# Optimization experiments

Measured on AMD Instinct MI355X. Metric: run time of the kernel, lower is better.

## Reference

```python
import jax, jax.numpy as jnp
import numpy as np

S = 2048      # seq_len
E = 1024      # embedding_size
H = 16        # attn_head
D = E // H    # per-head dim = 64
EPS = 1e-5


def _layernorm(x, g, b):
    mu = jnp.mean(x, axis=-1, keepdims=True)
    var = jnp.var(x, axis=-1, keepdims=True)
    return (x - mu) * jax.lax.rsqrt(var + EPS) * g + b


def setup_inputs() -> dict:
    key = jax.random.key(0)
    ks = jax.random.split(key, 16)
    s = 1.0 / np.sqrt(E)
    inp = {
        "x_word_emb": jax.random.normal(ks[0], (S, E), jnp.float32),
        "x_pos_emb": jax.random.normal(ks[1], (S, E), jnp.float32),
        # stacked per-head projections: weight [H, E, D], bias [H, D]
        "Wq": jax.random.uniform(ks[2], (H, E, D), jnp.float32, -s, s),
        "bq": jax.random.uniform(ks[3], (H, D), jnp.float32, -s, s),
        "Wk": jax.random.uniform(ks[4], (H, E, D), jnp.float32, -s, s),
        "bk": jax.random.uniform(ks[5], (H, D), jnp.float32, -s, s),
        "Wv": jax.random.uniform(ks[6], (H, E, D), jnp.float32, -s, s),
        "bv": jax.random.uniform(ks[7], (H, D), jnp.float32, -s, s),
        "W0": jax.random.uniform(ks[8], (E, E), jnp.float32, -s, s),
        "b0": jax.random.uniform(ks[9], (E,), jnp.float32, -s, s),
        "g1": jnp.ones((E,), jnp.float32),
        "be1": jnp.zeros((E,), jnp.float32),
        "W1": jax.random.uniform(ks[10], (4 * E, E), jnp.float32, -s, s),
        "b1": jax.random.uniform(ks[11], (4 * E,), jnp.float32, -s, s),
        "W2": jax.random.uniform(ks[12], (E, 4 * E), jnp.float32, -1.0 / np.sqrt(4 * E), 1.0 / np.sqrt(4 * E)),
        "b2": jax.random.uniform(ks[13], (E,), jnp.float32, -1.0 / np.sqrt(4 * E), 1.0 / np.sqrt(4 * E)),
        "g2": jnp.ones((E,), jnp.float32),
        "be2": jnp.zeros((E,), jnp.float32),
    }
    return inp


def reference(x_word_emb, x_pos_emb, Wq, bq, Wk, bk, Wv, bv,
              W0, b0, g1, be1, W1, b1, W2, b2, g2, be2):
    emb = x_word_emb + x_pos_emb                            # [S, E]
    # batched per-head projections (equivalent to the per-head Linear loop)
    q = jnp.einsum('se,hed->hsd', emb, Wq) + bq[:, None, :]  # [H, S, D]
    k = jnp.einsum('se,hed->hsd', emb, Wk) + bk[:, None, :]
    v = jnp.einsum('se,hed->hsd', emb, Wv) + bv[:, None, :]
    scores = jnp.einsum('hsd,htd->hst', q, k)               # [H, S, S]
    # original: F.softmax(z).data -> weights detached (no grad through q/k)
    w = jax.lax.stop_gradient(jax.nn.softmax(scores, axis=-1))
    # NOTE: original scales AFTER softmax@V, not on the logits
    z = jnp.einsum('hst,htd->hsd', w, v) / np.sqrt(D)       # [H, S, D]
    # concat heads along feature dim in head order
    z = jnp.transpose(z, (1, 0, 2)).reshape(S, E)           # [S, E]
    z = z @ W0.T + b0
    out1 = _layernorm(z + emb, g1, be1)
    out2 = jax.nn.relu(out1 @ W1.T + b1)                    # [S, 4E]
    out2 = out2 @ W2.T + b2
    return _layernorm(out1 + out2, g2, be2)
```

## Files before the change

### kernel.cpp

```cpp
#include <hip/hip_runtime.h>

#define SLEN 2048
#define EDIM 1024
#define HNUM 16
#define DDIM 64

typedef unsigned short u16;
typedef unsigned int u32;
typedef __attribute__((ext_vector_type(8))) __bf16 bf16x8;
typedef __attribute__((ext_vector_type(2))) __bf16 bf16x2;
typedef __attribute__((ext_vector_type(4))) float f32x4;
typedef __attribute__((ext_vector_type(16))) float f32x16;

__device__ __forceinline__ u16 f2bf(float f) {
  u32 u = __builtin_bit_cast(u32, f);
  u = (u + 0x7fffu + ((u >> 16) & 1u)) >> 16;
  return (u16)u;
}

__device__ __forceinline__ float bf2f(u16 v) {
  u32 u = ((u32)v) << 16;
  return __builtin_bit_cast(float, u);
}

__device__ __forceinline__ u32 packbf(float a, float b) {
  bf16x2 t; t[0] = (__bf16)a; t[1] = (__bf16)b;
  return __builtin_bit_cast(u32, t);
}

__device__ __forceinline__ void gload_lds16(const void* g, void* l) {
  __builtin_amdgcn_global_load_lds(
      (const __attribute__((address_space(1))) void*)g,
      (__attribute__((address_space(3))) void*)l, 16, 0, 0);
}

__device__ __forceinline__ u32 swz(u32 b) { return b ^ (((b >> 7) & 7u) << 4); }

template<int MODE>
__global__ __launch_bounds__(256, 2) void gemm_bt(
    const u16* __restrict__ A, const u16* __restrict__ Bt,
    const float* __restrict__ bias, const float* __restrict__ add,
    void* __restrict__ outp, int M, int N, int K)
{
  __shared__ __align__(16) u16 As[128 * 64];
  __shared__ __align__(16) u16 Bs[128 * 64];
  const int t = threadIdx.x;
  const int lane = t & 63, wv = t >> 6;
  const int bm = blockIdx.y * 128, bn = blockIdx.x * 128;
  const int wm = (wv >> 1) * 64, wn = (wv & 1) * 64;
  f32x4 acc[4][4] = {};

  const char* Ab = (const char*)A;
  const char* Bb = (const char*)Bt;

  for (int k0 = 0; k0 < K; k0 += 64) {
    __syncthreads();
#pragma unroll
    for (int j = 0; j < 4; ++j) {
      u32 bp = (u32)t * 16u + (u32)j * 4096u;
      u32 L = swz(bp);
      u32 row = L >> 7, colb = L & 127u;
      gload_lds16(Ab + ((size_t)(bm + row) * K + k0) * 2 + colb, (char*)As + bp);
      gload_lds16(Bb + ((size_t)(bn + row) * K + k0) * 2 + colb, (char*)Bs + bp);
    }
    __syncthreads();
#pragma unroll
    for (int ks = 0; ks < 2; ++ks) {
      bf16x8 af[4], bfr[4];
#pragma unroll
      for (int i = 0; i < 4; ++i) {
        u32 ra = (u32)(wm + i * 16 + (lane & 15));
        u32 La = (ra << 7) + (u32)ks * 64u + (u32)(lane >> 4) * 16u;
        af[i] = *(const bf16x8*)((const char*)As + (La ^ ((ra & 7u) << 4)));
        u32 rb = (u32)(wn + i * 16 + (lane & 15));
        u32 Lb = (rb << 7) + (u32)ks * 64u + (u32)(lane >> 4) * 16u;
        bfr[i] = *(const bf16x8*)((const char*)Bs + (Lb ^ ((rb & 7u) << 4)));
      }
#pragma unroll
      for (int mi = 0; mi < 4; ++mi)
#pragma unroll
        for (int ni = 0; ni < 4; ++ni)
          acc[mi][ni] = __builtin_amdgcn_mfma_f32_16x16x32_bf16(af[mi], bfr[ni], acc[mi][ni], 0, 0, 0);
    }
  }

  const int cr = (lane >> 4) * 4, cc = lane & 15;
#pragma unroll
  for (int ni = 0; ni < 4; ++ni) {
    const int col = bn + wn + ni * 16 + cc;
    const float bvv = bias[col];
#pragma unroll
    for (int mi = 0; mi < 4; ++mi) {
#pragma unroll
      for (int r = 0; r < 4; ++r) {
        const int row = bm + wm + mi * 16 + cr + r;
        float v = acc[mi][ni][r] + bvv;
        const size_t idx = (size_t)row * N + col;
        if constexpr (MODE == 0) ((u16*)outp)[idx] = f2bf(v);
        else if constexpr (MODE == 1) ((u16*)outp)[idx] = f2bf(v > 0.f ? v : 0.f);
        else ((float*)outp)[idx] = v + add[idx];
      }
    }
  }
}

template<int MODE>
__global__ __launch_bounds__(256, 4) void gemm_bt64(
    const u16* __restrict__ A, const u16* __restrict__ Bt,
    const float* __restrict__ bias, float* __restrict__ part1,
    void* __restrict__ outp, int M, int N, int lda, int KS)
{
  __shared__ __align__(16) u16 As[64 * 64];
  __shared__ __align__(16) u16 Bs[128 * 64];
  const int t = threadIdx.x;
  const int lane = t & 63, wv = t >> 6;
  const int bm = blockIdx.y * 64, bn = blockIdx.x * 128;
  const int wm = (wv >> 1) * 32, wn = (wv & 1) * 64;
  const int koff = blockIdx.z * KS;
  f32x4 acc[2][4] = {};

  const char* Ab = (const char*)A;
  const char* Bb = (const char*)Bt;

  for (int k0 = koff; k0 < koff + KS; k0 += 64) {
    __syncthreads();
    {
      u32 bp = (u32)t * 16u;
      u32 L = swz(bp);
      u32 row = L >> 7, colb = L & 127u;
      gload_lds16(Ab + ((size_t)(bm + row) * lda + k0) * 2 + colb, (char*)As + bp);
      u32 bp2 = bp + 4096u;
      u32 L2 = swz(bp2);
      u32 row2 = L2 >> 7, colb2 = L2 & 127u;
      gload_lds16(Ab + ((size_t)(bm + row2) * lda + k0) * 2 + colb2, (char*)As + bp2);
    }
#pragma unroll
    for (int j = 0; j < 4; ++j) {
      u32 bp = (u32)t * 16u + (u32)j * 4096u;
      u32 L = swz(bp);
      u32 row = L >> 7, colb = L & 127u;
      gload_lds16(Bb + ((size_t)(bn + row) * lda + k0) * 2 + colb, (char*)Bs + bp);
    }
    __syncthreads();
#pragma unroll
    for (int ks = 0; ks < 2; ++ks) {
      bf16x8 af[2], bfr[4];
#pragma unroll
      for (int i = 0; i < 2; ++i) {
        u32 ra = (u32)(wm + i * 16 + (lane & 15));
        u32 La = (ra << 7) + (u32)ks * 64u + (u32)(lane >> 4) * 16u;
        af[i] = *(const bf16x8*)((const char*)As + (La ^ ((ra & 7u) << 4)));
      }
#pragma unroll
      for (int i = 0; i < 4; ++i) {
        u32 rb = (u32)(wn + i * 16 + (lane & 15));
        u32 Lb = (rb << 7) + (u32)ks * 64u + (u32)(lane >> 4) * 16u;
        bfr[i] = *(const bf16x8*)((const char*)Bs + (Lb ^ ((rb & 7u) << 4)));
      }
#pragma unroll
      for (int mi = 0; mi < 2; ++mi)
#pragma unroll
        for (int ni = 0; ni < 4; ++ni)
          acc[mi][ni] = __builtin_amdgcn_mfma_f32_16x16x32_bf16(af[mi], bfr[ni], acc[mi][ni], 0, 0, 0);
    }
  }

  float* po = (MODE == 3 && blockIdx.z) ? part1 : (float*)outp;
  const int cr = (lane >> 4) * 4, cc = lane & 15;
#pragma unroll
  for (int ni = 0; ni < 4; ++ni) {
    const int col = bn + wn + ni * 16 + cc;
    const float bvv = (MODE == 3) ? 0.f : bias[col];
#pragma unroll
    for (int mi = 0; mi < 2; ++mi) {
#pragma unroll
      for (int r = 0; r < 4; ++r) {
        const int row = bm + wm + mi * 16 + cr + r;
        float v = acc[mi][ni][r] + bvv;
        const size_t idx = (size_t)row * N + col;
        if constexpr (MODE == 0) ((u16*)outp)[idx] = f2bf(v);
        else if constexpr (MODE == 1) ((u16*)outp)[idx] = f2bf(v > 0.f ? v : 0.f);
        else po[idx] = v;
      }
    }
  }
}

__global__ __launch_bounds__(256, 4) void attn_kernel(
    const u16* __restrict__ qkv, const u16* __restrict__ vt,
    u16* __restrict__ zp, float2* __restrict__ mlb)
{
  __shared__ __align__(16) char lds[32768];
  const int t = threadIdx.x, lane = t & 63;
  const int q31 = lane & 31, hi = lane >> 5;
  const int wv = t >> 6;
  const int h = blockIdx.y;
  const int qrow = blockIdx.x * 128 + wv * 32 + q31;
  const int kt0 = blockIdx.z * 12;
  const int cnt = (blockIdx.z == 2) ? 8 : 12;

  bf16x8 qf[4];
#pragma unroll
  for (int ds = 0; ds < 4; ++ds)
    qf[ds] = *(const bf16x8*)(qkv + (size_t)qrow * 3072 + h * 64 + ds * 16 + hi * 8);

  const char* kgp[2];
  const char* vgp[2];
  u32 ldo[2];
#pragma unroll
  for (int j = 0; j < 2; ++j) {
    u32 bp = (u32)t * 16u + (u32)j * 4096u;
    u32 L = swz(bp);
    u32 row = L >> 7, colb = L & 127u;
    kgp[j] = (const char*)qkv + ((size_t)row * 3072 + 1024 + h * 64) * 2 + colb;
    vgp[j] = (const char*)vt + ((size_t)(h * 64 + row)) * (SLEN * 2) + colb;
    ldo[j] = bp;
  }

  f32x16 zacc[2] = {};
  float m = -1e30f, l = 0.f;

  {
    size_t ko = (size_t)kt0 * (64 * 3072 * 2);
    int vo = kt0 * 128;
#pragma unroll
    for (int j = 0; j < 2; ++j) {
      gload_lds16(kgp[j] + ko, lds + ldo[j]);
      gload_lds16(vgp[j] + vo, lds + 8192 + ldo[j]);
    }
  }
  __syncthreads();

  int cur = 0;
  for (int it = 0; it < cnt; ++it) {
    const int kt = kt0 + it;
    if (it + 1 < cnt) {
      char* base = lds + (cur ^ 1) * 16384;
      size_t ko = (size_t)(kt + 1) * (64 * 3072 * 2);
      int vo = (kt + 1) * 128;
#pragma unroll
      for (int j = 0; j < 2; ++j) {
        gload_lds16(kgp[j] + ko, base + ldo[j]);
        gload_lds16(vgp[j] + vo, base + 8192 + ldo[j]);
      }
    }

    const char* Kl = lds + cur * 16384;
    const char* Vl = Kl + 8192;

#pragma unroll
    for (int kh = 0; kh < 2; ++kh) {
      f32x16 p = {};
#pragma unroll
      for (int ds = 0; ds < 4; ++ds) {
        u32 rk = (u32)(kh * 32 + q31);
        u32 L = (rk << 7) + (u32)ds * 32u + (u32)hi * 16u;
        bf16x8 kf = *(const bf16x8*)(Kl + (L ^ ((rk & 7u) << 4)));
        p = __builtin_amdgcn_mfma_f32_32x32x16_bf16(kf, qf[ds], p, 0, 0, 0);
      }

      float tmax = p[0];
#pragma unroll
      for (int r = 1; r < 16; ++r) tmax = fmaxf(tmax, p[r]);
      tmax = fmaxf(tmax, __shfl_xor(tmax, 32));
      if (!__all(tmax <= m)) {
        float newm = fmaxf(m, tmax);
        float scl = __expf(m - newm);
        l *= scl;
#pragma unroll
        for (int r = 0; r < 16; ++r) { zacc[0][r] *= scl; zacc[1][r] *= scl; }
        m = newm;
      }
      float psum = 0.f;
      u32 w[8];
#pragma unroll
      for (int j = 0; j < 8; ++j) {
        float e0 = __expf(p[2 * j] - m);
        float e1 = __expf(p[2 * j + 1] - m);
        psum += e0 + e1;
        w[j] = packbf(e0, e1);
      }
      psum += __shfl_xor(psum, 32);
      l += psum;

#pragma unroll
      for (int ktl = 0; ktl < 2; ++ktl) {
        u32 A0 = w[4 * ktl + 0], B0 = w[4 * ktl + 2];
        asm volatile("v_permlane32_swap_b32 %0, %1" : "+v"(A0), "+v"(B0));
        u32 A1 = w[4 * ktl + 1], B1 = w[4 * ktl + 3];
        asm volatile("v_permlane32_swap_b32 %0, %1" : "+v"(A1), "+v"(B1));
        uint4 pw = {A0, A1, B0, B1};
        bf16x8 pf = __builtin_bit_cast(bf16x8, pw);
#pragma unroll
        for (int dh = 0; dh < 2; ++dh) {
          u32 rv = (u32)(dh * 32 + q31);
          u32 L = (rv << 7) + (u32)(kh * 64 + ktl * 32) + (u32)hi * 16u;
          bf16x8 vf = *(const bf16x8*)(Vl + (L ^ ((rv & 7u) << 4)));
          zacc[dh] = __builtin_amdgcn_mfma_f32_32x32x16_bf16(vf, pf, zacc[dh], 0, 0, 0);
        }
      }
    }
    __syncthreads();
    cur ^= 1;
  }

  const int bid = (h * 16 + blockIdx.x) * 3 + blockIdx.z;
  u16* zb = zp + (size_t)bid * 8192 + (size_t)(wv * 32 + q31) * 64;
#pragma unroll
  for (int dh = 0; dh < 2; ++dh)
#pragma unroll
    for (int g = 0; g < 4; ++g) {
      int d0 = dh * 32 + g * 8 + hi * 4;
      uint2 st;
      st.x = packbf(zacc[dh][4 * g + 0], zacc[dh][4 * g + 1]);
      st.y = packbf(zacc[dh][4 * g + 2], zacc[dh][4 * g + 3]);
      *(uint2*)(zb + d0) = st;
    }
  if (hi == 0) mlb[(size_t)bid * 128 + wv * 32 + q31] = make_float2(m, l);
}

__global__ __launch_bounds__(256) void comb_kernel(
    const u16* __restrict__ zp, const float2* __restrict__ mlb, u16* __restrict__ zcat)
{
  const int flat = blockIdx.x * 256 + threadIdx.x;
  const int d4 = flat & 15;
  const int q = (flat >> 4) & 2047;
  const int h = flat >> 15;
  const int qt = q >> 7, qr = q & 127;
  const size_t pb = (size_t)(h * 16 + qt) * 3;
  const size_t base = pb * 8192 + (size_t)qr * 64 + d4 * 4;
  uint2 a = *(const uint2*)(zp + base);
  uint2 b = *(const uint2*)(zp + base + 8192);
  uint2 c = *(const uint2*)(zp + base + 16384);
  float2 ml0 = mlb[pb * 128 + qr];
  float2 ml1 = mlb[(pb + 1) * 128 + qr];
  float2 ml2 = mlb[(pb + 2) * 128 + qr];
  const float M = fmaxf(fmaxf(ml0.x, ml1.x), ml2.x);
  const float e0 = __expf(ml0.x - M), e1 = __expf(ml1.x - M), e2 = __expf(ml2.x - M);
  const float s = 0.125f / (e0 * ml0.y + e1 * ml1.y + e2 * ml2.y);
  float o0 = (e0 * bf2f((u16)(a.x & 0xffff)) + e1 * bf2f((u16)(b.x & 0xffff)) + e2 * bf2f((u16)(c.x & 0xffff))) * s;
  float o1 = (e0 * bf2f((u16)(a.x >> 16))   + e1 * bf2f((u16)(b.x >> 16))   + e2 * bf2f((u16)(c.x >> 16))) * s;
  float o2 = (e0 * bf2f((u16)(a.y & 0xffff)) + e1 * bf2f((u16)(b.y & 0xffff)) + e2 * bf2f((u16)(c.y & 0xffff))) * s;
  float o3 = (e0 * bf2f((u16)(a.y >> 16))   + e1 * bf2f((u16)(b.y >> 16))   + e2 * bf2f((u16)(c.y >> 16))) * s;
  uint2 st;
  st.x = (u32)f2bf(o0) | ((u32)f2bf(o1) << 16);
  st.y = (u32)f2bf(o2) | ((u32)f2bf(o3) << 16);
  *(uint2*)(zcat + (size_t)q * EDIM + h * 64 + d4 * 4) = st;
}

__global__ __launch_bounds__(256) void lnred_kernel(
    const float4* __restrict__ pA, const float4* __restrict__ pB,
    const float* __restrict__ bias, const float4* __restrict__ add,
    const float* __restrict__ g, const float* __restrict__ b,
    float* __restrict__ outf, u16* __restrict__ outb)
{
  const int row = blockIdx.x, t = threadIdx.x;
  const int i = row * 256 + t;
  float4 a = pA[i], p2 = pB[i], c = add[i];
  float4 bs = ((const float4*)bias)[t];
  float4 x;
  x.x = a.x + p2.x + c.x + bs.x;
  x.y = a.y + p2.y + c.y + bs.y;
  x.z = a.z + p2.z + c.z + bs.z;
  x.w = a.w + p2.w + c.w + bs.w;
  float s = x.x + x.y + x.z + x.w;
  float sq = x.x * x.x + x.y * x.y + x.z * x.z + x.w * x.w;
#pragma unroll
  for (int msk = 1; msk < 64; msk <<= 1) { s += __shfl_xor(s, msk); sq += __shfl_xor(sq, msk); }
  __shared__ float red[8];
  const int wv = t >> 6, lane = t & 63;
  if (lane == 0) { red[wv] = s; red[4 + wv] = sq; }
  __syncthreads();
  s = red[0] + red[1] + red[2] + red[3];
  sq = red[4] + red[5] + red[6] + red[7];
  const float mu = s * (1.f / EDIM);
  const float rs = rsqrtf(sq * (1.f / EDIM) - mu * mu + 1e-5f);
  float4 gg = ((const float4*)g)[t];
  float4 bb = ((const float4*)b)[t];
  float4 y;
  y.x = (x.x - mu) * rs * gg.x + bb.x;
  y.y = (x.y - mu) * rs * gg.y + bb.y;
  y.z = (x.z - mu) * rs * gg.z + bb.z;
  y.w = (x.w - mu) * rs * gg.w + bb.w;
  if (outf) ((float4*)(outf + (size_t)row * EDIM))[t] = y;
  if (outb) {
    uint2 pkv;
    pkv.x = (u32)f2bf(y.x) | ((u32)f2bf(y.y) << 16);
    pkv.y = (u32)f2bf(y.z) | ((u32)f2bf(y.w) << 16);
    ((uint2*)(outb + (size_t)row * EDIM))[t] = pkv;
  }
}

__global__ void emb_kernel(const float4* __restrict__ a, const float4* __restrict__ b,
                           float4* __restrict__ ef, uint2* __restrict__ eb)
{
  const int i = blockIdx.x * 256 + threadIdx.x;
  float4 x = a[i], y = b[i];
  float4 e; e.x = x.x + y.x; e.y = x.y + y.y; e.z = x.z + y.z; e.w = x.w + y.w;
  ef[i] = e;
  uint2 pk;
  pk.x = (u32)f2bf(e.x) | ((u32)f2bf(e.y) << 16);
  pk.y = (u32)f2bf(e.z) | ((u32)f2bf(e.w) << 16);
  eb[i] = pk;
}

__global__ void cvt_kernel(const float4* __restrict__ in, uint2* __restrict__ out, int n4)
{
  const int i = blockIdx.x * 256 + threadIdx.x;
  if (i >= n4) return;
  float4 x = in[i];
  uint2 pk;
  pk.x = (u32)f2bf(x.x) | ((u32)f2bf(x.y) << 16);
  pk.y = (u32)f2bf(x.z) | ((u32)f2bf(x.w) << 16);
  out[i] = pk;
}

__global__ void bias3_kernel(const float* __restrict__ bq, const float* __restrict__ bk,
                             const float* __restrict__ bv, float* __restrict__ o)
{
  const int i = blockIdx.x * 256 + threadIdx.x;
  if (i >= 3072) return;
  o[i] = i < 1024 ? bq[i] : (i < 2048 ? bk[i - 1024] : bv[i - 2048]);
}

__global__ __launch_bounds__(256) void wqkv_kernel(
    const float* __restrict__ Wq, const float* __restrict__ Wk, const float* __restrict__ Wv,
    u16* __restrict__ outw)
{
  __shared__ float tile[64][65];
  const int et = blockIdx.x, h = blockIdx.y, wsel = blockIdx.z;
  const float* W = wsel == 0 ? Wq : (wsel == 1 ? Wk : Wv);
  const float* src = W + ((size_t)h * EDIM + et * 64) * DDIM;
  const int t = threadIdx.x;
#pragma unroll
  for (int it = 0; it < 4; ++it) {
    int fi = (t + it * 256) * 4;
    float4 v = *(const float4*)(src + fi);
    int e = fi >> 6, d = fi & 63;
    tile[e][d] = v.x; tile[e][d + 1] = v.y; tile[e][d + 2] = v.z; tile[e][d + 3] = v.w;
  }
  __syncthreads();
  const int d = t >> 2, ec = (t & 3) * 16;
  u16* dst = outw + ((size_t)(wsel * HNUM + h) * 64 + d) * EDIM + et * 64 + ec;
#pragma unroll
  for (int i = 0; i < 16; i += 2) {
    u32 p = (u32)f2bf(tile[ec + i][d]) | ((u32)f2bf(tile[ec + i + 1][d]) << 16);
    *(u32*)(dst + i) = p;
  }
}

__global__ __launch_bounds__(256) void vt_kernel(const u16* __restrict__ qkv, u16* __restrict__ vt)
{
  __shared__ __align__(16) u16 tile[64][80];
  const int st = blockIdx.x, h = blockIdx.y, t = threadIdx.x;
  const int sr = t >> 2, dc = (t & 3) * 16;
  const u16* src = qkv + (size_t)(st * 64 + sr) * 3072 + 2048 + h * 64 + dc;
  *(uint4*)&tile[sr][dc] = *(const uint4*)src;
  *(uint4*)&tile[sr][dc + 8] = *(const uint4*)(src + 8);
  __syncthreads();
  const int d = t >> 2, sc = (t & 3) * 16;
  u16* dst = vt + ((size_t)h * 64 + d) * SLEN + st * 64 + sc;
#pragma unroll
  for (int i = 0; i < 16; i += 2) {
    u32 p = (u32)tile[sc + i][d] | ((u32)tile[sc + i + 1][d] << 16);
    *(u32*)(dst + i) = p;
  }
}

extern "C" void kernel_launch(void* const* d_in, const int* in_sizes, int n_in,
                              void* d_out, int out_size, void* d_ws, size_t ws_size,
                              hipStream_t stream) {
  const float* xw  = (const float*)d_in[0];
  const float* xp  = (const float*)d_in[1];
  const float* Wq  = (const float*)d_in[2];
  const float* bq  = (const float*)d_in[3];
  const float* Wk  = (const float*)d_in[4];
  const float* bk  = (const float*)d_in[5];
  const float* Wv  = (const float*)d_in[6];
  const float* bv  = (const float*)d_in[7];
  const float* W0  = (const float*)d_in[8];
  const float* b0  = (const float*)d_in[9];
  const float* g1  = (const float*)d_in[10];
  const float* be1 = (const float*)d_in[11];
  const float* W1  = (const float*)d_in[12];
  const float* b1  = (const float*)d_in[13];
  const float* W2  = (const float*)d_in[14];
  const float* b2  = (const float*)d_in[15];
  const float* g2  = (const float*)d_in[16];
  const float* be2 = (const float*)d_in[17];
  float* out = (float*)d_out;
  char* ws = (char*)d_ws;

  const size_t MB = 1ull << 20;
  float* embf32 = (float*)(ws + 0);
  u16*   embf16 = (u16*)(ws + 8 * MB);
  u16*   zcat   = (u16*)(ws + 8 * MB);
  u16*   out1b  = (u16*)(ws + 8 * MB);
  u16*   Wqkvt  = (u16*)(ws + 12 * MB);
  float2* mlb   = (float2*)(ws + 12 * MB);
  u16*   h1     = (u16*)(ws + 12 * MB);
  u16*   QKV    = (u16*)(ws + 18 * MB);
  float* w0pA   = (float*)(ws + 18 * MB);
  float* w0pB   = (float*)(ws + 26 * MB);
  u16*   Vt     = (u16*)(ws + 30 * MB);
  u16*   zp     = (u16*)(ws + 34 * MB);
  float* out1f  = (float*)(ws + 34 * MB);
  u16*   W0b    = (u16*)(ws + 46 * MB);
  u16*   W1b    = (u16*)(ws + 48 * MB);
  u16*   W2b    = (u16*)(ws + 56 * MB);
  float* w2pA   = (float*)(ws + 0);
  float* w2pB   = (float*)(ws + 42 * MB);
  float* bias3  = (float*)(ws + 64 * MB);

  emb_kernel<<<2048, 256, 0, stream>>>((const float4*)xw, (const float4*)xp,
                                       (float4*)embf32, (uint2*)embf16);
  cvt_kernel<<<1024, 256, 0, stream>>>((const float4*)W0, (uint2*)W0b, 1024 * 1024 / 4);
  cvt_kernel<<<4096, 256, 0, stream>>>((const float4*)W1, (uint2*)W1b, 4096 * 1024 / 4);
  cvt_kernel<<<4096, 256, 0, stream>>>((const float4*)W2, (uint2*)W2b, 1024 * 4096 / 4);
  bias3_kernel<<<12, 256, 0, stream>>>(bq, bk, bv, bias3);
  wqkv_kernel<<<dim3(16, 16, 3), 256, 0, stream>>>(Wq, Wk, Wv, Wqkvt);

  gemm_bt64<0><<<dim3(3072 / 128, 2048 / 64, 1), 256, 0, stream>>>(
      embf16, Wqkvt, bias3, nullptr, QKV, SLEN, 3072, 1024, 1024);

  vt_kernel<<<dim3(32, 16), 256, 0, stream>>>(QKV, Vt);

  attn_kernel<<<dim3(SLEN / 128, HNUM, 3), 256, 0, stream>>>(QKV, Vt, zp, mlb);
  comb_kernel<<<2048, 256, 0, stream>>>(zp, mlb, zcat);

  gemm_bt64<3><<<dim3(1024 / 128, 2048 / 64, 2), 256, 0, stream>>>(
      zcat, W0b, nullptr, w0pB, w0pA, SLEN, 1024, 1024, 512);
  lnred_kernel<<<SLEN, 256, 0, stream>>>((const float4*)w0pA, (const float4*)w0pB,
                                         b0, (const float4*)embf32, g1, be1, out1f, out1b);

  gemm_bt<1><<<dim3(4096 / 128, 2048 / 128), 256, 0, stream>>>(
      out1b, W1b, b1, nullptr, h1, SLEN, 4096, 1024);

  gemm_bt64<3><<<dim3(1024 / 128, 2048 / 64, 2), 256, 0, stream>>>(
      h1, W2b, nullptr, w2pB, w2pA, SLEN, 1024, 4096, 2048);
  lnred_kernel<<<SLEN, 256, 0, stream>>>((const float4*)w2pA, (const float4*)w2pB,
                                         b2, (const float4*)out1f, g2, be2, out, nullptr);
}
```

Measured before the change: 169.3 us.

## Double-buffer LDS tiles in GEMM kernels and remap block order for L2 locality

Both GEMM kernels now keep two LDS buffers and prefetch the next K tile with async global-to-LDS loads while MFMAs run on the current tile, leaving one barrier per iteration instead of two. The block index is also remapped in strides of 8 so neighbouring blocks share A/B tiles in cache. Swizzle addresses are precomputed once outside the loop. LDS use doubles, so gemm_bt64 occupancy drops from 4 to 3 blocks and gemm_bt may be limited by LDS. The remap assumes the grid size is divisible by 8.

```diff
diff --git a/kernel.cpp b/kernel.cpp
--- a/kernel.cpp
+++ b/kernel.cpp
@@ -42,28 +42,47 @@
     const float* __restrict__ bias, const float* __restrict__ add,
     void* __restrict__ outp, int M, int N, int K)
 {
-  __shared__ __align__(16) u16 As[128 * 64];
-  __shared__ __align__(16) u16 Bs[128 * 64];
+  __shared__ __align__(16) u16 As[2][128 * 64];
+  __shared__ __align__(16) u16 Bs[2][128 * 64];
   const int t = threadIdx.x;
-  const int lane = t & 63, wv = t >> 6;
-  const int bm = blockIdx.y * 128, bn = blockIdx.x * 128;
+  const int lane = t & 63;
+  const u32 nxy = gridDim.x * gridDim.y;
+  u32 lid = blockIdx.y * gridDim.x + blockIdx.x;
+  lid = (lid & 7u) * (nxy >> 3) + (lid >> 3);
+  const int bxx = lid % gridDim.x, byy = lid / gridDim.x;
+  const int bm = byy * 128, bn = bxx * 128;
+  const int wv = t >> 6;
   const int wm = (wv >> 1) * 64, wn = (wv & 1) * 64;
   f32x4 acc[4][4] = {};
 
   const char* Ab = (const char*)A;
   const char* Bb = (const char*)Bt;
 
+  u32 srow[4], scol[4], sdst[4];
+#pragma unroll
+  for (int j = 0; j < 4; ++j) {
+    u32 bp = (u32)t * 16u + (u32)j * 4096u;
+    u32 L = swz(bp);
+    srow[j] = L >> 7; scol[j] = L & 127u; sdst[j] = bp;
+  }
+
+#pragma unroll
+  for (int j = 0; j < 4; ++j) {
+    gload_lds16(Ab + ((size_t)(bm + srow[j]) * K) * 2 + scol[j], (char*)As[0] + sdst[j]);
+    gload_lds16(Bb + ((size_t)(bn + srow[j]) * K) * 2 + scol[j], (char*)Bs[0] + sdst[j]);
+  }
+  __syncthreads();
+
+  int cur = 0;
   for (int k0 = 0; k0 < K; k0 += 64) {
-    __syncthreads();
-#pragma unroll
-    for (int j = 0; j < 4; ++j) {
-      u32 bp = (u32)t * 16u + (u32)j * 4096u;
-      u32 L = swz(bp);
-      u32 row = L >> 7, colb = L & 127u;
-      gload_lds16(Ab + ((size_t)(bm + row) * K + k0) * 2 + colb, (char*)As + bp);
-      gload_lds16(Bb + ((size_t)(bn + row) * K + k0) * 2 + colb, (char*)Bs + bp);
-    }
-    __syncthreads();
+    const int nxt = k0 + 64;
+    if (nxt < K) {
+#pragma unroll
+      for (int j = 0; j < 4; ++j) {
+        gload_lds16(Ab + ((size_t)(bm + srow[j]) * K + nxt) * 2 + scol[j], (char*)As[cur ^ 1] + sdst[j]);
+        gload_lds16(Bb + ((size_t)(bn + srow[j]) * K + nxt) * 2 + scol[j], (char*)Bs[cur ^ 1] + sdst[j]);
+      }
+    }
 #pragma unroll
     for (int ks = 0; ks < 2; ++ks) {
       bf16x8 af[4], bfr[4];
@@ -71,10 +90,10 @@
       for (int i = 0; i < 4; ++i) {
         u32 ra = (u32)(wm + i * 16 + (lane & 15));
         u32 La = (ra << 7) + (u32)ks * 64u + (u32)(lane >> 4) * 16u;
-        af[i] = *(const bf16x8*)((const char*)As + (La ^ ((ra & 7u) << 4)));
+        af[i] = *(const bf16x8*)((const char*)As[cur] + (La ^ ((ra & 7u) << 4)));
         u32 rb = (u32)(wn + i * 16 + (lane & 15));
         u32 Lb = (rb << 7) + (u32)ks * 64u + (u32)(lane >> 4) * 16u;
-        bfr[i] = *(const bf16x8*)((const char*)Bs + (Lb ^ ((rb & 7u) << 4)));
+        bfr[i] = *(const bf16x8*)((const char*)Bs[cur] + (Lb ^ ((rb & 7u) << 4)));
       }
 #pragma unroll
       for (int mi = 0; mi < 4; ++mi)
@@ -82,6 +101,8 @@
         for (int ni = 0; ni < 4; ++ni)
           acc[mi][ni] = __builtin_amdgcn_mfma_f32_16x16x32_bf16(af[mi], bfr[ni], acc[mi][ni], 0, 0, 0);
     }
+    __syncthreads();
+    cur ^= 1;
   }
 
   const int cr = (lane >> 4) * 4, cc = lane & 15;
@@ -105,16 +126,21 @@
 }
 
 template<int MODE>
-__global__ __launch_bounds__(256, 4) void gemm_bt64(
+__global__ __launch_bounds__(256, 3) void gemm_bt64(
     const u16* __restrict__ A, const u16* __restrict__ Bt,
     const float* __restrict__ bias, float* __restrict__ part1,
     void* __restrict__ outp, int M, int N, int lda, int KS)
 {
-  __shared__ __align__(16) u16 As[64 * 64];
-  __shared__ __align__(16) u16 Bs[128 * 64];
+  __shared__ __align__(16) u16 As[2][64 * 64];
+  __shared__ __align__(16) u16 Bs[2][128 * 64];
   const int t = threadIdx.x;
-  const int lane = t & 63, wv = t >> 6;
-  const int bm = blockIdx.y * 64, bn = blockIdx.x * 128;
+  const int lane = t & 63;
+  const u32 nxy = gridDim.x * gridDim.y;
+  u32 lid = blockIdx.y * gridDim.x + blockIdx.x;
+  lid = (lid & 7u) * (nxy >> 3) + (lid >> 3);
+  const int bxx = lid % gridDim.x, byy = lid / gridDim.x;
+  const int bm = byy * 64, bn = bxx * 128;
+  const int wv = t >> 6;
   const int wm = (wv >> 1) * 32, wn = (wv & 1) * 64;
   const int koff = blockIdx.z * KS;
   f32x4 acc[2][4] = {};
@@ -122,26 +148,33 @@
   const char* Ab = (const char*)A;
   const char* Bb = (const char*)Bt;
 
+  u32 srow[4], scol[4], sdst[4];
+#pragma unroll
+  for (int j = 0; j < 4; ++j) {
+    u32 bp = (u32)t * 16u + (u32)j * 4096u;
+    u32 L = swz(bp);
+    srow[j] = L >> 7; scol[j] = L & 127u; sdst[j] = bp;
+  }
+
+#pragma unroll
+  for (int j = 0; j < 2; ++j)
+    gload_lds16(Ab + ((size_t)(bm + srow[j]) * lda + koff) * 2 + scol[j], (char*)As[0] + sdst[j]);
+#pragma unroll
+  for (int j = 0; j < 4; ++j)
+    gload_lds16(Bb + ((size_t)(bn + srow[j]) * lda + koff) * 2 + scol[j], (char*)Bs[0] + sdst[j]);
+  __syncthreads();
+
+  int cur = 0;
   for (int k0 = koff; k0 < koff + KS; k0 += 64) {
-    __syncthreads();
-    {
-      u32 bp = (u32)t * 16u;
-      u32 L = swz(bp);
-      u32 row = L >> 7, colb = L & 127u;
-      gload_lds16(Ab + ((size_t)(bm + row) * lda + k0) * 2 + colb, (char*)As + bp);
-      u32 bp2 = bp + 4096u;
-      u32 L2 = swz(bp2);
-      u32 row2 = L2 >> 7, colb2 = L2 & 127u;
-      gload_lds16(Ab + ((size_t)(bm + row2) * lda + k0) * 2 + colb2, (char*)As + bp2);
-    }
-#pragma unroll
-    for (int j = 0; j < 4; ++j) {
-      u32 bp = (u32)t * 16u + (u32)j * 4096u;
-      u32 L = swz(bp);
-      u32 row = L >> 7, colb = L & 127u;
-      gload_lds16(Bb + ((size_t)(bn + row) * lda + k0) * 2 + colb, (char*)Bs + bp);
-    }
-    __syncthreads();
+    const int nxt = k0 + 64;
+    if (nxt < koff + KS) {
+#pragma unroll
+      for (int j = 0; j < 2; ++j)
+        gload_lds16(Ab + ((size_t)(bm + srow[j]) * lda + nxt) * 2 + scol[j], (char*)As[cur ^ 1] + sdst[j]);
+#pragma unroll
+      for (int j = 0; j < 4; ++j)
+        gload_lds16(Bb + ((size_t)(bn + srow[j]) * lda + nxt) * 2 + scol[j], (char*)Bs[cur ^ 1] + sdst[j]);
+    }
 #pragma unroll
     for (int ks = 0; ks < 2; ++ks) {
       bf16x8 af[2], bfr[4];
@@ -149,13 +182,13 @@
       for (int i = 0; i < 2; ++i) {
         u32 ra = (u32)(wm + i * 16 + (lane & 15));
         u32 La = (ra << 7) + (u32)ks * 64u + (u32)(lane >> 4) * 16u;
-        af[i] = *(const bf16x8*)((const char*)As + (La ^ ((ra & 7u) << 4)));
+        af[i] = *(const bf16x8*)((const char*)As[cur] + (La ^ ((ra & 7u) << 4)));
       }
 #pragma unroll
       for (int i = 0; i < 4; ++i) {
         u32 rb = (u32)(wn + i * 16 + (lane & 15));
         u32 Lb = (rb << 7) + (u32)ks * 64u + (u32)(lane >> 4) * 16u;
-        bfr[i] = *(const bf16x8*)((const char*)Bs + (Lb ^ ((rb & 7u) << 4)));
+        bfr[i] = *(const bf16x8*)((const char*)Bs[cur] + (Lb ^ ((rb & 7u) << 4)));
       }
 #pragma unroll
       for (int mi = 0; mi < 2; ++mi)
@@ -163,6 +196,8 @@
         for (int ni = 0; ni < 4; ++ni)
           acc[mi][ni] = __builtin_amdgcn_mfma_f32_16x16x32_bf16(af[mi], bfr[ni], acc[mi][ni], 0, 0, 0);
     }
+    __syncthreads();
+    cur ^= 1;
   }
 
   float* po = (MODE == 3 && blockIdx.z) ? part1 : (float*)outp;
```

Result: slower. 172.8 us (+2.1%).

## Merge preprocessing kernels and write transposed V directly from QKV GEMM epilogue

Applied to the files above, without the earlier changes.

Combines the embedding add, weight bf16 conversions, QKV weight transpose and bias concat into a single prep kernel dispatched by block index, cutting several launches. The QKV GEMM epilogue now writes V columns directly into the transposed Vt layout, removing the separate vt_kernel pass over V. The transposed stores are strided 8-byte writes, which may be less coalesced than the original row-major stores.

```diff
diff --git a/kernel.cpp b/kernel.cpp
--- a/kernel.cpp
+++ b/kernel.cpp
@@ -108,7 +108,7 @@
 __global__ __launch_bounds__(256, 4) void gemm_bt64(
     const u16* __restrict__ A, const u16* __restrict__ Bt,
     const float* __restrict__ bias, float* __restrict__ part1,
-    void* __restrict__ outp, int M, int N, int lda, int KS)
+    void* __restrict__ outp, u16* __restrict__ vtp, int M, int N, int lda, int KS)
 {
   __shared__ __align__(16) u16 As[64 * 64];
   __shared__ __align__(16) u16 Bs[128 * 64];
@@ -169,18 +169,32 @@
   const int cr = (lane >> 4) * 4, cc = lane & 15;
 #pragma unroll
   for (int ni = 0; ni < 4; ++ni) {
-    const int col = bn + wn + ni * 16 + cc;
-    const float bvv = (MODE == 3) ? 0.f : bias[col];
-#pragma unroll
-    for (int mi = 0; mi < 2; ++mi) {
-#pragma unroll
-      for (int r = 0; r < 4; ++r) {
-        const int row = bm + wm + mi * 16 + cr + r;
-        float v = acc[mi][ni][r] + bvv;
-        const size_t idx = (size_t)row * N + col;
-        if constexpr (MODE == 0) ((u16*)outp)[idx] = f2bf(v);
-        else if constexpr (MODE == 1) ((u16*)outp)[idx] = f2bf(v > 0.f ? v : 0.f);
-        else po[idx] = v;
+    const int colb0 = bn + wn + ni * 16;
+    const int col = colb0 + cc;
+    if (MODE == 0 && vtp != nullptr && colb0 >= 2048) {
+      const float bvv = bias[col];
+      const int vcol = col - 2048;
+#pragma unroll
+      for (int mi = 0; mi < 2; ++mi) {
+        const int row0 = bm + wm + mi * 16 + cr;
+        uint2 st;
+        st.x = packbf(acc[mi][ni][0] + bvv, acc[mi][ni][1] + bvv);
+        st.y = packbf(acc[mi][ni][2] + bvv, acc[mi][ni][3] + bvv);
+        *(uint2*)(vtp + (size_t)vcol * SLEN + row0) = st;
+      }
+    } else {
+      const float bvv = (MODE == 3) ? 0.f : bias[col];
+#pragma unroll
+      for (int mi = 0; mi < 2; ++mi) {
+#pragma unroll
+        for (int r = 0; r < 4; ++r) {
+          const int row = bm + wm + mi * 16 + cr + r;
+          float v = acc[mi][ni][r] + bvv;
+          const size_t idx = (size_t)row * N + col;
+          if constexpr (MODE == 0) ((u16*)outp)[idx] = f2bf(v);
+          else if constexpr (MODE == 1) ((u16*)outp)[idx] = f2bf(v > 0.f ? v : 0.f);
+          else po[idx] = v;
+        }
       }
     }
   }
@@ -391,79 +405,61 @@
   }
 }
 
-__global__ void emb_kernel(const float4* __restrict__ a, const float4* __restrict__ b,
-                           float4* __restrict__ ef, uint2* __restrict__ eb)
-{
-  const int i = blockIdx.x * 256 + threadIdx.x;
-  float4 x = a[i], y = b[i];
-  float4 e; e.x = x.x + y.x; e.y = x.y + y.y; e.z = x.z + y.z; e.w = x.w + y.w;
-  ef[i] = e;
-  uint2 pk;
-  pk.x = (u32)f2bf(e.x) | ((u32)f2bf(e.y) << 16);
-  pk.y = (u32)f2bf(e.z) | ((u32)f2bf(e.w) << 16);
-  eb[i] = pk;
-}
-
-__global__ void cvt_kernel(const float4* __restrict__ in, uint2* __restrict__ out, int n4)
-{
-  const int i = blockIdx.x * 256 + threadIdx.x;
-  if (i >= n4) return;
-  float4 x = in[i];
-  uint2 pk;
-  pk.x = (u32)f2bf(x.x) | ((u32)f2bf(x.y) << 16);
-  pk.y = (u32)f2bf(x.z) | ((u32)f2bf(x.w) << 16);
-  out[i] = pk;
-}
-
-__global__ void bias3_kernel(const float* __restrict__ bq, const float* __restrict__ bk,
-                             const float* __restrict__ bv, float* __restrict__ o)
-{
-  const int i = blockIdx.x * 256 + threadIdx.x;
-  if (i >= 3072) return;
-  o[i] = i < 1024 ? bq[i] : (i < 2048 ? bk[i - 1024] : bv[i - 2048]);
-}
-
-__global__ __launch_bounds__(256) void wqkv_kernel(
+__global__ __launch_bounds__(256) void prep_kernel(
+    const float4* __restrict__ xw, const float4* __restrict__ xp,
+    float4* __restrict__ embf32, uint2* __restrict__ embf16,
+    const float4* __restrict__ W0, const float4* __restrict__ W1, const float4* __restrict__ W2,
+    uint2* __restrict__ W0b, uint2* __restrict__ W1b, uint2* __restrict__ W2b,
     const float* __restrict__ Wq, const float* __restrict__ Wk, const float* __restrict__ Wv,
-    u16* __restrict__ outw)
+    u16* __restrict__ Wqkvt,
+    const float* __restrict__ bq, const float* __restrict__ bk, const float* __restrict__ bv,
+    float* __restrict__ bias3)
 {
   __shared__ float tile[64][65];
-  const int et = blockIdx.x, h = blockIdx.y, wsel = blockIdx.z;
-  const float* W = wsel == 0 ? Wq : (wsel == 1 ? Wk : Wv);
-  const float* src = W + ((size_t)h * EDIM + et * 64) * DDIM;
-  const int t = threadIdx.x;
-#pragma unroll
-  for (int it = 0; it < 4; ++it) {
-    int fi = (t + it * 256) * 4;
-    float4 v = *(const float4*)(src + fi);
-    int e = fi >> 6, d = fi & 63;
-    tile[e][d] = v.x; tile[e][d + 1] = v.y; tile[e][d + 2] = v.z; tile[e][d + 3] = v.w;
-  }
-  __syncthreads();
-  const int d = t >> 2, ec = (t & 3) * 16;
-  u16* dst = outw + ((size_t)(wsel * HNUM + h) * 64 + d) * EDIM + et * 64 + ec;
-#pragma unroll
-  for (int i = 0; i < 16; i += 2) {
-    u32 p = (u32)f2bf(tile[ec + i][d]) | ((u32)f2bf(tile[ec + i + 1][d]) << 16);
-    *(u32*)(dst + i) = p;
-  }
-}
-
-__global__ __launch_bounds__(256) void vt_kernel(const u16* __restrict__ qkv, u16* __restrict__ vt)
-{
-  __shared__ __align__(16) u16 tile[64][80];
-  const int st = blockIdx.x, h = blockIdx.y, t = threadIdx.x;
-  const int sr = t >> 2, dc = (t & 3) * 16;
-  const u16* src = qkv + (size_t)(st * 64 + sr) * 3072 + 2048 + h * 64 + dc;
-  *(uint4*)&tile[sr][dc] = *(const uint4*)src;
-  *(uint4*)&tile[sr][dc + 8] = *(const uint4*)(src + 8);
-  __syncthreads();
-  const int d = t >> 2, sc = (t & 3) * 16;
-  u16* dst = vt + ((size_t)h * 64 + d) * SLEN + st * 64 + sc;
-#pragma unroll
-  for (int i = 0; i < 16; i += 2) {
-    u32 p = (u32)tile[sc + i][d] | ((u32)tile[sc + i + 1][d] << 16);
-    *(u32*)(dst + i) = p;
+  const int b = blockIdx.x, t = threadIdx.x;
+  if (b < 2048) {
+    const int i = b * 256 + t;
+    float4 x = xw[i], y = xp[i];
+    float4 e; e.x = x.x + y.x; e.y = x.y + y.y; e.z = x.z + y.z; e.w = x.w + y.w;
+    embf32[i] = e;
+    uint2 pk;
+    pk.x = (u32)f2bf(e.x) | ((u32)f2bf(e.y) << 16);
+    pk.y = (u32)f2bf(e.z) | ((u32)f2bf(e.w) << 16);
+    embf16[i] = pk;
+  } else if (b < 11264) {
+    const int i = (b - 2048) * 256 + t;
+    float4 x; uint2* dst;
+    if (i < 262144) { x = W0[i]; dst = W0b + i; }
+    else if (i < 1310720) { int j = i - 262144; x = W1[j]; dst = W1b + j; }
+    else { int j = i - 1310720; x = W2[j]; dst = W2b + j; }
+    uint2 pk;
+    pk.x = (u32)f2bf(x.x) | ((u32)f2bf(x.y) << 16);
+    pk.y = (u32)f2bf(x.z) | ((u32)f2bf(x.w) << 16);
+    *dst = pk;
+  } else if (b < 12032) {
+    const int idx = b - 11264;
+    const int et = idx & 15, h = (idx >> 4) & 15, wsel = idx >> 8;
+    const float* W = wsel == 0 ? Wq : (wsel == 1 ? Wk : Wv);
+    const float* src = W + ((size_t)h * EDIM + et * 64) * DDIM;
+#pragma unroll
+    for (int it = 0; it < 4; ++it) {
+      int fi = (t + it * 256) * 4;
+      float4 v = *(const float4*)(src + fi);
+      int e = fi >> 6, d = fi & 63;
+      tile[e][d] = v.x; tile[e][d + 1] = v.y; tile[e][d + 2] = v.z; tile[e][d + 3] = v.w;
+    }
+    __syncthreads();
+    const int d = t >> 2, ec = (t & 3) * 16;
+    u16* dst = Wqkvt + ((size_t)(wsel * HNUM + h) * 64 + d) * EDIM + et * 64 + ec;
+#pragma unroll
+    for (int i = 0; i < 16; i += 2) {
+      u32 p = (u32)f2bf(tile[ec + i][d]) | ((u32)f2bf(tile[ec + i + 1][d]) << 16);
+      *(u32*)(dst + i) = p;
+    }
+  } else {
+    const int i = (b - 12032) * 256 + t;
+    if (i < 3072)
+      bias3[i] = i < 1024 ? bq[i] : (i < 2048 ? bk[i - 1024] : bv[i - 2048]);
   }
 }
 
@@ -512,24 +508,20 @@
   float* w2pB   = (float*)(ws + 42 * MB);
   float* bias3  = (float*)(ws + 64 * MB);
 
-  emb_kernel<<<2048, 256, 0, stream>>>((const float4*)xw, (const float4*)xp,
-                                       (float4*)embf32, (uint2*)embf16);
-  cvt_kernel<<<1024, 256, 0, stream>>>((const float4*)W0, (uint2*)W0b, 1024 * 1024 / 4);
-  cvt_kernel<<<4096, 256, 0, stream>>>((const float4*)W1, (uint2*)W1b, 4096 * 1024 / 4);
-  cvt_kernel<<<4096, 256, 0, stream>>>((const float4*)W2, (uint2*)W2b, 1024 * 4096 / 4);
-  bias3_kernel<<<12, 256, 0, stream>>>(bq, bk, bv, bias3);
-  wqkv_kernel<<<dim3(16, 16, 3), 256, 0, stream>>>(Wq, Wk, Wv, Wqkvt);
+  prep_kernel<<<12044, 256, 0, stream>>>(
+      (const float4*)xw, (const float4*)xp, (float4*)embf32, (uint2*)embf16,
+      (const float4*)W0, (const float4*)W1, (const float4*)W2,
+      (uint2*)W0b, (uint2*)W1b, (uint2*)W2b,
+      Wq, Wk, Wv, Wqkvt, bq, bk, bv, bias3);
 
   gemm_bt64<0><<<dim3(3072 / 128, 2048 / 64, 1), 256, 0, stream>>>(
-      embf16, Wqkvt, bias3, nullptr, QKV, SLEN, 3072, 1024, 1024);
-
-  vt_kernel<<<dim3(32, 16), 256, 0, stream>>>(QKV, Vt);
+      embf16, Wqkvt, bias3, nullptr, QKV, Vt, SLEN, 3072, 1024, 1024);
 
   attn_kernel<<<dim3(SLEN / 128, HNUM, 3), 256, 0, stream>>>(QKV, Vt, zp, mlb);
   comb_kernel<<<2048, 256, 0, stream>>>(zp, mlb, zcat);
 
   gemm_bt64<3><<<dim3(1024 / 128, 2048 / 64, 2), 256, 0, stream>>>(
-      zcat, W0b, nullptr, w0pB, w0pA, SLEN, 1024, 1024, 512);
+      zcat, W0b, nullptr, w0pB, w0pA, nullptr, SLEN, 1024, 1024, 512);
   lnred_kernel<<<SLEN, 256, 0, stream>>>((const float4*)w0pA, (const float4*)w0pB,
                                          b0, (const float4*)embf32, g1, be1, out1f, out1b);
 
@@ -537,7 +529,7 @@
       out1b, W1b, b1, nullptr, h1, SLEN, 4096, 1024);
 
   gemm_bt64<3><<<dim3(1024 / 128, 2048 / 64, 2), 256, 0, stream>>>(
-      h1, W2b, nullptr, w2pB, w2pA, SLEN, 1024, 4096, 2048);
+      h1, W2b, nullptr, w2pB, w2pA, nullptr, SLEN, 1024, 4096, 2048);
   lnred_kernel<<<SLEN, 256, 0, stream>>>((const float4*)w2pA, (const float4*)w2pB,
                                          b2, (const float4*)out1f, g2, be2, out, nullptr);
 }
```

New measurement: 160.1 us. 1.06x faster.
